# Performance work log

Measured on AMD Instinct MI355X. Metric: run time of the kernel, lower is better.

## Reference

```python
import jax, jax.numpy as jnp
import numpy as np
from jax import lax

# ---- constants matching init kwargs / proposal_creator(mode='testing') ----
RATIOS = (0.5, 1.0, 2.0)
SCALES = (8.0, 16.0, 32.0)
BASE = 16.0          # generate_anchor_base base_size
STRIDE = 16          # feat_stride
NMS_THRESH = 0.7
N_PRE = 3000         # n_test_pre_nms
N_POST = 300         # n_test_post_nms
MIN_SIZE = 16.0      # min_size * scale (scale=1)


def _anchor_base():
    # (9, 4) xyxy anchors centered at (BASE/2, BASE/2); ratios outer, scales inner
    r = np.array(RATIOS, np.float32)
    s = np.array(SCALES, np.float32)
    hs = (BASE * s[None, :] * np.sqrt(r)[:, None]).reshape(-1)
    ws = (BASE * s[None, :] * np.sqrt(1.0 / r)[:, None]).reshape(-1)
    cx = cy = BASE / 2.0
    return np.stack([cx - ws / 2, cy - hs / 2, cx + ws / 2, cy + hs / 2], 1).astype(np.float32)


def _all_anchors(h, w):
    # _enumerate_shifted_anchor: shift grid flattened y-outer/x-inner to match
    # permute(0,2,3,1).view(n,-1,4) layout of the conv outputs.
    base = jnp.asarray(_anchor_base())                     # (9,4)
    sx = jnp.arange(w, dtype=jnp.float32) * STRIDE
    sy = jnp.arange(h, dtype=jnp.float32) * STRIDE
    SX, SY = jnp.meshgrid(sx, sy)                          # (h,w)
    shifts = jnp.stack([SX, SY, SX, SY], -1).reshape(-1, 4)  # (h*w,4)
    return (shifts[:, None, :] + base[None, :, :]).reshape(-1, 4)  # (h*w*9,4)


def _proposals(loc, score, anchor, img_h, img_w):
    # loc: (K,4) deltas, score: (K,) fg prob, anchor: (K,4) xyxy
    aw = anchor[:, 2] - anchor[:, 0]
    ah = anchor[:, 3] - anchor[:, 1]
    acx = anchor[:, 0] + 0.5 * aw
    acy = anchor[:, 1] + 0.5 * ah
    cx = loc[:, 0] * aw + acx
    cy = loc[:, 1] * ah + acy
    bw = aw * jnp.exp(loc[:, 2])
    bh = ah * jnp.exp(loc[:, 3])
    x1 = jnp.clip(cx - 0.5 * bw, 0.0, img_w)
    y1 = jnp.clip(cy - 0.5 * bh, 0.0, img_h)
    x2 = jnp.clip(cx + 0.5 * bw, 0.0, img_w)
    y2 = jnp.clip(cy + 0.5 * bh, 0.0, img_h)
    boxes = jnp.stack([x1, y1, x2, y2], 1)
    valid = ((x2 - x1) >= MIN_SIZE) & ((y2 - y1) >= MIN_SIZE)
    # min-size filter -> sink invalid boxes with -inf score, then top-k pre-NMS
    masked = jnp.where(valid, score, -jnp.inf)
    _, idx = lax.top_k(masked, N_PRE)
    b = boxes[idx]                                         # (N_PRE,4), score-sorted desc
    v = valid[idx]
    # pairwise IoU (torchvision convention: no +1)
    area = (b[:, 2] - b[:, 0]) * (b[:, 3] - b[:, 1])
    ix1 = jnp.maximum(b[:, None, 0], b[None, :, 0])
    iy1 = jnp.maximum(b[:, None, 1], b[None, :, 1])
    ix2 = jnp.minimum(b[:, None, 2], b[None, :, 2])
    iy2 = jnp.minimum(b[:, None, 3], b[None, :, 3])
    inter = jnp.clip(ix2 - ix1, 0.0) * jnp.clip(iy2 - iy1, 0.0)
    union = area[:, None] + area[None, :] - inter
    iou = jnp.where(union > 0.0, inter / union, 0.0)
    sup = iou > NMS_THRESH                                 # (N_PRE,N_PRE) bool
    # greedy sequential NMS over score order
    ar = jnp.arange(N_PRE)
    def body(keep, i):
        keep = keep & ~(keep[i] & sup[i] & (ar > i))
        return keep, None
    keep, _ = lax.scan(body, v, ar)
    # first N_POST kept boxes (score order); pad by cycling kept boxes
    order = jnp.argsort(jnp.where(keep, ar, N_PRE))        # kept indices first, sorted
    nk = jnp.maximum(keep.sum(), 1)
    pos = jnp.arange(N_POST)
    sel = order[jnp.where(pos < nk, pos, pos % nk)]
    return b[sel]                                          # (N_POST,4)


def setup_inputs() -> dict:
    key = jax.random.key(0)
    ks = jax.random.split(key, 4)
    n, c, h, w = 4, 512, 38, 38
    return {
        "x": jax.random.normal(ks[0], (n, c, h, w), jnp.float32),
        "conv1_w": jax.random.normal(ks[1], (512, 512, 3, 3), jnp.float32) * 0.01,
        "conv1_b": jnp.zeros((512,), jnp.float32),
        "score_w": jax.random.normal(ks[2], (18, 512), jnp.float32) * 0.01,
        "score_b": jnp.zeros((18,), jnp.float32),
        "loc_w": jax.random.normal(ks[3], (36, 512), jnp.float32) * 0.01,
        "loc_b": jnp.zeros((36,), jnp.float32),
        "img_h": 608,
        "img_w": 608,
    }


def reference(x, conv1_w, conv1_b, score_w, score_b, loc_w, loc_b, img_h, img_w):
    n, _, h, w = x.shape
    feat = jax.nn.relu(
        lax.conv_general_dilated(x, conv1_w, (1, 1), "SAME",
                                 dimension_numbers=("NCHW", "OIHW", "NCHW"))
        + conv1_b[None, :, None, None])
    locs = jnp.einsum("nchw,oc->nohw", feat, loc_w) + loc_b[None, :, None, None]
    scores = jnp.einsum("nchw,oc->nohw", feat, score_w) + score_b[None, :, None, None]
    rpn_locs = locs.transpose(0, 2, 3, 1).reshape(n, -1, 4)      # (n, h*w*9, 4)
    rpn_scores = scores.transpose(0, 2, 3, 1).reshape(n, -1, 2)  # (n, h*w*9, 2)
    fg = jax.nn.softmax(rpn_scores, axis=-1)[..., 1]             # (n, h*w*9)
    anchor = _all_anchors(h, w)
    ih = jnp.float32(img_h)
    iw = jnp.float32(img_w)
    rois = jax.vmap(lambda l, s: _proposals(l, s, anchor, ih, iw))(rpn_locs, fg)
    rois_indices = jnp.broadcast_to(
        jnp.arange(n, dtype=x.dtype)[:, None], (n, N_POST))
    return rpn_locs, rpn_scores, rois.reshape(-1, 4), rois_indices, anchor[None]
```

## Files before the change

kernel.cpp:

```cpp
#include <hip/hip_runtime.h>
#include <cstdint>
#include <cstddef>

#define HW    1444
#define NA    12996
#define NPRE  3000
#define NW    47
#define NPOST 300

#define OFF_LOCS   0
#define OFF_SCORES 207936
#define OFF_ROIS   311904
#define OFF_IDX    316704
#define OFF_ANCH   317904

#define INVALID_KEY 0xFFF0000000000000ULL

__device__ inline double as_dim(int raw) {
  if (raw > 0 && raw < 1000000) return (double)raw;
  return (double)__int_as_float(raw);
}

__global__ __launch_bounds__(256) void wt_k(const float* __restrict__ lw,
                                            const float* __restrict__ sw,
                                            float* __restrict__ Wt) {
  int t = blockIdx.x * 256 + threadIdx.x;
  if (t >= 64 * 512) return;
  int o = t & 63, c = t >> 6;
  float v = 0.f;
  if (o < 36)      v = lw[o * 512 + c];
  else if (o < 54) v = sw[(o - 36) * 512 + c];
  Wt[t] = v;
}

__global__ __launch_bounds__(256) void conv_k(const float* __restrict__ X,
                                              const float* __restrict__ W,
                                              const float* __restrict__ B,
                                              float* __restrict__ F) {
  __shared__ float Xs[480];
  __shared__ float Wsf[2340];
  const int tid  = threadIdx.x;
  const int lane = tid & 63;
  const int wv   = tid >> 6;
  const int seg  = wv * 10;
  const int y  = blockIdx.x;
  const int o0 = blockIdx.y * 64;
  const int n  = blockIdx.z;
  const float* xn = X + ((size_t)n * 512) * HW;

  int xsrc[2]; bool xval[2]; bool xact[2];
#pragma unroll
  for (int u = 0; u < 2; ++u) {
    int e = tid + u * 256;
    xact[u] = (e < 480);
    int cl = e / 120, rem = e - cl * 120;
    int row = rem / 40, col = rem - row * 40;
    int iy = y - 1 + row, ix = col - 1;
    xval[u] = xact[u] && (iy >= 0 && iy < 38 && ix >= 0 && ix < 38);
    xsrc[u] = xval[u] ? (cl * HW + iy * 38 + ix) : 0;
  }
  int wdst[9], wsrc[9];
#pragma unroll
  for (int u = 0; u < 9; ++u) {
    int e = tid + u * 256;
    int ol = e / 36, rem = e - ol * 36;
    int cl = rem / 9, k = rem - cl * 9;
    wdst[u] = (cl * 9 + k) * 65 + ol;
    wsrc[u] = (o0 + ol) * 4608 + cl * 9 + k;
  }

  float xr_[2], wr_[9];
#pragma unroll
  for (int u = 0; u < 2; ++u) xr_[u] = xval[u] ? xn[xsrc[u]] : 0.f;
#pragma unroll
  for (int u = 0; u < 9; ++u) wr_[u] = W[wsrc[u]];

  double acc[10];
#pragma unroll
  for (int p = 0; p < 10; ++p) acc[p] = 0.;
  float part[10];

  for (int cc = 0; cc < 128; ++cc) {
    __syncthreads();
#pragma unroll
    for (int u = 0; u < 2; ++u)
      if (xact[u]) Xs[tid + u * 256] = xr_[u];
#pragma unroll
    for (int u = 0; u < 9; ++u) Wsf[wdst[u]] = wr_[u];
    __syncthreads();
    if (cc < 127) {
      const int cb = (cc + 1) * 4;
#pragma unroll
      for (int u = 0; u < 2; ++u) xr_[u] = xval[u] ? xn[(size_t)cb * HW + xsrc[u]] : 0.f;
#pragma unroll
      for (int u = 0; u < 9; ++u) wr_[u] = W[wsrc[u] + cb * 9];
    }
    if ((cc & 1) == 0) {
#pragma unroll
      for (int p = 0; p < 10; ++p) part[p] = 0.f;
    }
#pragma unroll
    for (int cl = 0; cl < 4; ++cl) {
      float w9[9];
#pragma unroll
      for (int k = 0; k < 9; ++k) w9[k] = Wsf[(cl * 9 + k) * 65 + lane];
#pragma unroll
      for (int ky = 0; ky < 3; ++ky) {
        const float* xrow = &Xs[cl * 120 + ky * 40 + seg];
        float xr[12];
#pragma unroll
        for (int j = 0; j < 6; ++j) {
          float2 t2 = ((const float2*)xrow)[j];
          xr[2 * j] = t2.x; xr[2 * j + 1] = t2.y;
        }
#pragma unroll
        for (int kx = 0; kx < 3; ++kx) {
          float wvv = w9[ky * 3 + kx];
#pragma unroll
          for (int p = 0; p < 10; ++p)
            part[p] = fmaf(wvv, xr[p + kx], part[p]);
        }
      }
    }
    if (cc & 1) {
#pragma unroll
      for (int p = 0; p < 10; ++p) acc[p] += (double)part[p];
    }
  }
  double bb = (double)B[o0 + lane];
  float* fp = F + ((size_t)(n * 512 + o0 + lane)) * HW + y * 38;
#pragma unroll
  for (int p = 0; p < 10; ++p) {
    int col = seg + p;
    if (col < 38) fp[col] = (float)fmax(acc[p] + bb, 0.0);
  }
}

__global__ __launch_bounds__(256) void heads_k(const float* __restrict__ F,
                                               const float* __restrict__ Wt,
                                               const float* __restrict__ lb,
                                               const float* __restrict__ sb,
                                               float* __restrict__ out,
                                               double* __restrict__ fg) {
  __shared__ float sf[512 * 4];
  __shared__ double ssc[4][18];
  int n = blockIdx.y;
  int p0 = blockIdx.x * 4;
  int tid = threadIdx.x;
  const float* fn = F + ((size_t)n * 512) * HW;
  for (int e = tid; e < 2048; e += 256) {
    int c = e >> 2, pl = e & 3;
    sf[e] = fn[c * HW + p0 + pl];
  }
  __syncthreads();
  int pl = tid & 3, o = tid >> 2;
  double acc = 0.;
  if (o < 54) {
    for (int c = 0; c < 512; ++c)
      acc = fma((double)Wt[(c << 6) | o], (double)sf[(c << 2) | pl], acc);
  }
  int p = p0 + pl;
  if (o < 36) {
    acc += (double)lb[o];
    out[OFF_LOCS + ((size_t)n * NA + (size_t)p * 9 + (o >> 2)) * 4 + (o & 3)] = (float)acc;
  } else if (o < 54) {
    int oo = o - 36;
    acc += (double)sb[oo];
    out[OFF_SCORES + ((size_t)n * NA + (size_t)p * 9 + (oo >> 1)) * 2 + (oo & 1)] = (float)acc;
    ssc[pl][oo] = acc;
  }
  __syncthreads();
  if (tid < 36) {
    int pl2 = tid / 9, a = tid - pl2 * 9;
    double s0 = ssc[pl2][a * 2], s1 = ssc[pl2][a * 2 + 1];
    double mx = fmax(s0, s1);
    double e0 = exp(s0 - mx), e1 = exp(s1 - mx);
    fg[(size_t)n * NA + (size_t)(p0 + pl2) * 9 + a] = e1 / (e0 + e1);
  }
}

__global__ __launch_bounds__(256) void decode_k(const float* __restrict__ out_c,
                                                float* __restrict__ out,
                                                const double* __restrict__ fg,
                                                const int* __restrict__ ihp,
                                                const int* __restrict__ iwp,
                                                double* __restrict__ boxes,
                                                unsigned long long* __restrict__ keys) {
  int t = blockIdx.x * 256 + threadIdx.x;
  int n = t >> 14, i = t & 16383;
  if (i >= NA) { keys[t] = ~0ULL; return; }
  int p = i / 9, a = i - p * 9;
  int ri = a / 3, si = a - ri * 3;
  double sr  = (ri == 0) ? 0.7071067811865476 : (ri == 1 ? 1.0 : 1.4142135623730951);
  double sri = (ri == 0) ? 1.4142135623730951 : (ri == 1 ? 1.0 : 0.7071067811865476);
  double hs = (double)(128 << si) * sr;
  double wd = (double)(128 << si) * sri;
  int py = p / 38, px = p - py * 38;
  float sx = (float)(px * 16), sy = (float)(py * 16);
  float fx1 = (float)(8.0 - 0.5 * wd), fy1 = (float)(8.0 - 0.5 * hs);
  float fx2 = (float)(8.0 + 0.5 * wd), fy2 = (float)(8.0 + 0.5 * hs);
  float ax1f = sx + fx1, ay1f = sy + fy1, ax2f = sx + fx2, ay2f = sy + fy2;
  if (n == 0) {
    float* ap = out + OFF_ANCH + (size_t)i * 4;
    ap[0] = ax1f; ap[1] = ay1f; ap[2] = ax2f; ap[3] = ay2f;
  }
  double ax1 = ax1f, ay1 = ay1f, ax2 = ax2f, ay2 = ay2f;
  double aw = ax2 - ax1, ah = ay2 - ay1;
  double acx = ax1 + 0.5 * aw, acy = ay1 + 0.5 * ah;
  const float* lp = out_c + OFF_LOCS + ((size_t)n * NA + i) * 4;
  double cx = (double)lp[0] * aw + acx, cy = (double)lp[1] * ah + acy;
  double bw = aw * exp((double)lp[2]), bh = ah * exp((double)lp[3]);
  double iwf = as_dim(iwp[0]), ihf = as_dim(ihp[0]);
  double x1 = fmin(fmax(cx - 0.5 * bw, 0.0), iwf);
  double y1 = fmin(fmax(cy - 0.5 * bh, 0.0), ihf);
  double x2 = fmin(fmax(cx + 0.5 * bw, 0.0), iwf);
  double y2 = fmin(fmax(cy + 0.5 * bh, 0.0), ihf);
  bool valid = ((x2 - x1) >= 16.0) && ((y2 - y1) >= 16.0);
  double* bp = boxes + ((size_t)n * NA + i) * 4;
  bp[0] = x1; bp[1] = y1; bp[2] = x2; bp[3] = y2;
  double sc = fg[(size_t)n * NA + i];
  unsigned long long u = (unsigned long long)__double_as_longlong(sc);
  u = (u >> 63) ? ~u : (u | 0x8000000000000000ULL);
  unsigned long long inv = ~u;
  if (!valid) inv = INVALID_KEY;
  keys[t] = (inv & ~0x3FFFULL) | (unsigned long long)i;
}

__global__ __launch_bounds__(1024) void sortA_k(unsigned long long* __restrict__ keys) {
  __shared__ unsigned long long s[8192];
  const int half = blockIdx.x & 1;
  unsigned long long* g = keys + (((size_t)(blockIdx.x >> 1)) << 14) + ((size_t)half << 13);
  const int tid = threadIdx.x;
  for (int i = tid; i < 8192; i += 1024) s[i] = g[i];
  for (int size = 2; size <= 8192; size <<= 1) {
    for (int stride = size >> 1; stride > 0; stride >>= 1) {
      __syncthreads();
      for (int u = tid; u < 4096; u += 1024) {
        int lo = u & (stride - 1);
        int i1 = ((u - lo) << 1) | lo;
        int i2 = i1 + stride;
        bool up = (i1 & size) == 0;
        if (half) up = !up;
        unsigned long long a = s[i1], b = s[i2];
        if ((a > b) == up) { s[i1] = b; s[i2] = a; }
      }
    }
  }
  __syncthreads();
  for (int i = tid; i < 8192; i += 1024) g[i] = s[i];
}

__global__ __launch_bounds__(256) void sortB_k(unsigned long long* __restrict__ keys) {
  int t = blockIdx.x * 256 + threadIdx.x;
  int n = t >> 13, i = t & 8191;
  unsigned long long* g = keys + ((size_t)n << 14);
  unsigned long long a = g[i], b = g[i + 8192];
  if (a > b) { g[i] = b; g[i + 8192] = a; }
}

__global__ __launch_bounds__(1024) void sortC_k(unsigned long long* __restrict__ keys) {
  __shared__ unsigned long long s[8192];
  unsigned long long* g = keys + (((size_t)(blockIdx.x >> 1)) << 14) + ((size_t)(blockIdx.x & 1) << 13);
  const int tid = threadIdx.x;
  for (int i = tid; i < 8192; i += 1024) s[i] = g[i];
  for (int stride = 4096; stride > 0; stride >>= 1) {
    __syncthreads();
    for (int u = tid; u < 4096; u += 1024) {
      int lo = u & (stride - 1);
      int i1 = ((u - lo) << 1) | lo;
      int i2 = i1 + stride;
      unsigned long long a = s[i1], b = s[i2];
      if (a > b) { s[i1] = b; s[i2] = a; }
    }
  }
  __syncthreads();
  for (int i = tid; i < 8192; i += 1024) g[i] = s[i];
}

__global__ void gather_k(const unsigned long long* __restrict__ keys,
                         const double* __restrict__ boxes,
                         double* __restrict__ bsort,
                         unsigned long long* __restrict__ vw) {
  int n = blockIdx.y, w = blockIdx.x, l = threadIdx.x;
  int r = w * 64 + l;
  bool valid = false;
  if (r < NPRE) {
    unsigned long long kk = keys[((size_t)n << 14) + r];
    valid = kk < INVALID_KEY;
    unsigned idx = (unsigned)(kk & 0x3FFFULL);
    const double* bp = boxes + ((size_t)n * NA + idx) * 4;
    double* dp = bsort + ((size_t)n * NPRE + r) * 4;
    dp[0] = bp[0]; dp[1] = bp[1]; dp[2] = bp[2]; dp[3] = bp[3];
  }
  unsigned long long mask = __ballot(valid);
  if (l == 0) vw[n * NW + w] = mask;
}

__global__ __launch_bounds__(256) void iou_k(const double* __restrict__ bsort,
                                             unsigned long long* __restrict__ sup) {
  int t = blockIdx.x * 256 + threadIdx.x;
  if (t >= 4 * NPRE * NW) return;
  int w = t % NW; int rest = t / NW; int i = rest % NPRE; int n = rest / NPRE;
  const double* bb = bsort + (size_t)n * NPRE * 4;
  double bix1 = bb[(size_t)i*4], biy1 = bb[(size_t)i*4+1];
  double bix2 = bb[(size_t)i*4+2], biy2 = bb[(size_t)i*4+3];
  double ai = (bix2 - bix1) * (biy2 - biy1);
  unsigned long long word = 0ULL;
  int j0 = w << 6;
  if (j0 + 63 > i) {
    int lmax = NPRE - j0; if (lmax > 64) lmax = 64;
    for (int l = 0; l < lmax; ++l) {
      int j = j0 + l;
      if (j <= i) continue;
      const double* bj = bb + (size_t)j * 4;
      double aj = (bj[2] - bj[0]) * (bj[3] - bj[1]);
      double xx1 = fmax(bix1, bj[0]), yy1 = fmax(biy1, bj[1]);
      double xx2 = fmin(bix2, bj[2]), yy2 = fmin(biy2, bj[3]);
      double inter = fmax(xx2 - xx1, 0.0) * fmax(yy2 - yy1, 0.0);
      double uni = ai + aj - inter;
      double iou = (uni > 0.0) ? inter / uni : 0.0;
      word |= (unsigned long long)(iou > 0.7) << l;
    }
  }
  sup[((size_t)n * NPRE + i) * NW + w] = word;
}

__global__ void nms_k(const unsigned long long* __restrict__ sup,
                      const unsigned long long* __restrict__ vwp,
                      const double* __restrict__ bsort,
                      float* __restrict__ out) {
  int n = blockIdx.x; int l = threadIdx.x;
  unsigned long long vw = (l < NW) ? vwp[n * NW + l] : 0ULL;
  unsigned long long remv = 0ULL, keepw = 0ULL;
  const unsigned long long* sbase = sup + (size_t)n * NPRE * NW;
  unsigned long long r = (l < NPRE) ? sbase[(size_t)l * NW] : 0ULL;
  for (int b = 0; b < NW; ++b) {
    unsigned long long rn = 0ULL;
    if (b + 1 < NW) {
      int gi = (b + 1) * 64 + l;
      if (gi < NPRE) rn = sbase[(size_t)gi * NW + (b + 1)];
    }
    unsigned long long kept = __shfl(vw & ~remv, b);
    unsigned long long todo = kept;
    while (todo) {
      int i = __builtin_ctzll(todo);
      unsigned long long ri = __shfl(r, i);
      kept &= ~ri;
      todo &= todo - 1;
      todo &= ~ri;
    }
    if (l == b) keepw = kept;
    unsigned long long m = kept;
    while (m) {
      int i0 = __builtin_ctzll(m); m &= m - 1;
      int i1 = -1, i2 = -1, i3 = -1, i4 = -1, i5 = -1, i6 = -1, i7 = -1;
      if (m) { i1 = __builtin_ctzll(m); m &= m - 1; }
      if (m) { i2 = __builtin_ctzll(m); m &= m - 1; }
      if (m) { i3 = __builtin_ctzll(m); m &= m - 1; }
      if (m) { i4 = __builtin_ctzll(m); m &= m - 1; }
      if (m) { i5 = __builtin_ctzll(m); m &= m - 1; }
      if (m) { i6 = __builtin_ctzll(m); m &= m - 1; }
      if (m) { i7 = __builtin_ctzll(m); m &= m - 1; }
      if (l < NW) {
        const unsigned long long* rb = sbase + (size_t)(b << 6) * NW + l;
        unsigned long long a0 = rb[(size_t)i0 * NW];
        unsigned long long a1 = (i1 >= 0) ? rb[(size_t)i1 * NW] : 0ULL;
        unsigned long long a2 = (i2 >= 0) ? rb[(size_t)i2 * NW] : 0ULL;
        unsigned long long a3 = (i3 >= 0) ? rb[(size_t)i3 * NW] : 0ULL;
        unsigned long long a4 = (i4 >= 0) ? rb[(size_t)i4 * NW] : 0ULL;
        unsigned long long a5 = (i5 >= 0) ? rb[(size_t)i5 * NW] : 0ULL;
        unsigned long long a6 = (i6 >= 0) ? rb[(size_t)i6 * NW] : 0ULL;
        unsigned long long a7 = (i7 >= 0) ? rb[(size_t)i7 * NW] : 0ULL;
        remv |= (((a0 | a1) | (a2 | a3)) | ((a4 | a5) | (a6 | a7)));
      }
    }
    r = rn;
  }
  unsigned long long keep = keepw;
  int cnt = __popcll(keep);
  int pre = cnt;
#pragma unroll
  for (int d = 1; d < 64; d <<= 1) {
    int tt = __shfl_up(pre, d);
    if (l >= d) pre += tt;
  }
  int nk = __shfl(pre, 63);
  int excl = pre - cnt;
  __shared__ float sbox[NPOST * 4];
  unsigned long long m2 = keep; int rank = excl;
  while (m2) {
    int b = __builtin_ctzll(m2);
    m2 &= m2 - 1;
    if (rank < NPOST) {
      int j = (l << 6) + b;
      const double* bj = bsort + ((size_t)n * NPRE + j) * 4;
      sbox[rank*4]   = (float)bj[0]; sbox[rank*4+1] = (float)bj[1];
      sbox[rank*4+2] = (float)bj[2]; sbox[rank*4+3] = (float)bj[3];
    }
    ++rank;
  }
  __syncthreads();
  if (nk == 0 && l == 0) {
    const double* b0 = bsort + (size_t)n * NPRE * 4;
    sbox[0] = (float)b0[0]; sbox[1] = (float)b0[1];
    sbox[2] = (float)b0[2]; sbox[3] = (float)b0[3];
  }
  __syncthreads();
  int nke = nk > 0 ? nk : 1;
  for (int r2 = l; r2 < NPOST; r2 += 64) {
    int src = r2 < nke ? r2 : r2 % nke;
    float4 b4 = *(float4*)(sbox + src * 4);
    *(float4*)(out + OFF_ROIS + ((size_t)n * NPOST + r2) * 4) = b4;
    out[OFF_IDX + n * NPOST + r2] = (float)n;
  }
}

extern "C" void kernel_launch(void* const* d_in, const int* in_sizes, int n_in,
                              void* d_out, int out_size, void* d_ws, size_t ws_size,
                              hipStream_t stream) {
  const float* X  = (const float*)d_in[0];
  const float* CW = (const float*)d_in[1];
  const float* CB = (const float*)d_in[2];
  const float* SW = (const float*)d_in[3];
  const float* SB = (const float*)d_in[4];
  const float* LW = (const float*)d_in[5];
  const float* LB = (const float*)d_in[6];
  const int*   IH = (const int*)d_in[7];
  const int*   IW = (const int*)d_in[8];
  float* out = (float*)d_out;
  char* ws = (char*)d_ws;

  float* feat = (float*)(ws + 0);
  unsigned long long* sup  = (unsigned long long*)(ws + 0);
  float* Wt    = (float*)(ws + 11829248);
  double* fg   = (double*)(ws + 11960320);
  double* boxes= (double*)(ws + 12376192);
  unsigned long long* keys = (unsigned long long*)(ws + 14039680);
  double* bsort= (double*)(ws + 14563968);
  unsigned long long* vw   = (unsigned long long*)(ws + 14947968);

  hipLaunchKernelGGL(wt_k,     dim3(128),        dim3(256),  0, stream, LW, SW, Wt);
  hipLaunchKernelGGL(conv_k,   dim3(38, 8, 4),   dim3(256),  0, stream, X, CW, CB, feat);
  hipLaunchKernelGGL(heads_k,  dim3(361, 4),     dim3(256),  0, stream, feat, Wt, LB, SB, out, fg);
  hipLaunchKernelGGL(decode_k, dim3(256),        dim3(256),  0, stream, out, out, fg, IH, IW, boxes, keys);
  hipLaunchKernelGGL(sortA_k,  dim3(8),          dim3(1024), 0, stream, keys);
  hipLaunchKernelGGL(sortB_k,  dim3(128),        dim3(256),  0, stream, keys);
  hipLaunchKernelGGL(sortC_k,  dim3(8),          dim3(1024), 0, stream, keys);
  hipLaunchKernelGGL(gather_k, dim3(47, 4),      dim3(64),   0, stream, keys, boxes, bsort, vw);
  hipLaunchKernelGGL(iou_k,    dim3((4*NPRE*NW + 255) / 256), dim3(256), 0, stream, bsort, sup);
  hipLaunchKernelGGL(nms_k,    dim3(4),          dim3(64),   0, stream, sup, vw, bsort, out);
}
```

Baseline: 1.003 ms.

## Compute two output rows per conv block to reuse weights and input rows

```diff
diff --git a/kernel.cpp b/kernel.cpp
--- a/kernel.cpp
+++ b/kernel.cpp
@@ -37,25 +37,25 @@
                                               const float* __restrict__ W,
                                               const float* __restrict__ B,
                                               float* __restrict__ F) {
-  __shared__ float Xs[480];
+  __shared__ float Xs[640];
   __shared__ float Wsf[2340];
   const int tid  = threadIdx.x;
   const int lane = tid & 63;
   const int wv   = tid >> 6;
   const int seg  = wv * 10;
-  const int y  = blockIdx.x;
+  const int y0 = blockIdx.x * 2;
   const int o0 = blockIdx.y * 64;
   const int n  = blockIdx.z;
   const float* xn = X + ((size_t)n * 512) * HW;
 
-  int xsrc[2]; bool xval[2]; bool xact[2];
-#pragma unroll
-  for (int u = 0; u < 2; ++u) {
+  int xsrc[3]; bool xval[3]; bool xact[3];
+#pragma unroll
+  for (int u = 0; u < 3; ++u) {
     int e = tid + u * 256;
-    xact[u] = (e < 480);
-    int cl = e / 120, rem = e - cl * 120;
+    xact[u] = (e < 640);
+    int cl = e / 160, rem = e - cl * 160;
     int row = rem / 40, col = rem - row * 40;
-    int iy = y - 1 + row, ix = col - 1;
+    int iy = y0 - 1 + row, ix = col - 1;
     xval[u] = xact[u] && (iy >= 0 && iy < 38 && ix >= 0 && ix < 38);
     xsrc[u] = xval[u] ? (cl * HW + iy * 38 + ix) : 0;
   }
@@ -69,21 +69,23 @@
     wsrc[u] = (o0 + ol) * 4608 + cl * 9 + k;
   }
 
-  float xr_[2], wr_[9];
-#pragma unroll
-  for (int u = 0; u < 2; ++u) xr_[u] = xval[u] ? xn[xsrc[u]] : 0.f;
+  float xr_[3], wr_[9];
+#pragma unroll
+  for (int u = 0; u < 3; ++u) xr_[u] = xval[u] ? xn[xsrc[u]] : 0.f;
 #pragma unroll
   for (int u = 0; u < 9; ++u) wr_[u] = W[wsrc[u]];
 
-  double acc[10];
-#pragma unroll
-  for (int p = 0; p < 10; ++p) acc[p] = 0.;
-  float part[10];
+  double acc[2][10];
+#pragma unroll
+  for (int r = 0; r < 2; ++r)
+#pragma unroll
+    for (int p = 0; p < 10; ++p) acc[r][p] = 0.;
+  float part[2][10];
 
   for (int cc = 0; cc < 128; ++cc) {
     __syncthreads();
 #pragma unroll
-    for (int u = 0; u < 2; ++u)
+    for (int u = 0; u < 3; ++u)
       if (xact[u]) Xs[tid + u * 256] = xr_[u];
 #pragma unroll
     for (int u = 0; u < 9; ++u) Wsf[wdst[u]] = wr_[u];
@@ -91,48 +93,61 @@
     if (cc < 127) {
       const int cb = (cc + 1) * 4;
 #pragma unroll
-      for (int u = 0; u < 2; ++u) xr_[u] = xval[u] ? xn[(size_t)cb * HW + xsrc[u]] : 0.f;
+      for (int u = 0; u < 3; ++u) xr_[u] = xval[u] ? xn[(size_t)cb * HW + xsrc[u]] : 0.f;
 #pragma unroll
       for (int u = 0; u < 9; ++u) wr_[u] = W[wsrc[u] + cb * 9];
     }
     if ((cc & 1) == 0) {
 #pragma unroll
-      for (int p = 0; p < 10; ++p) part[p] = 0.f;
+      for (int r = 0; r < 2; ++r)
+#pragma unroll
+        for (int p = 0; p < 10; ++p) part[r][p] = 0.f;
     }
 #pragma unroll
     for (int cl = 0; cl < 4; ++cl) {
       float w9[9];
 #pragma unroll
       for (int k = 0; k < 9; ++k) w9[k] = Wsf[(cl * 9 + k) * 65 + lane];
-#pragma unroll
-      for (int ky = 0; ky < 3; ++ky) {
-        const float* xrow = &Xs[cl * 120 + ky * 40 + seg];
-        float xr[12];
+      float xr4[4][12];
+#pragma unroll
+      for (int rr = 0; rr < 4; ++rr) {
+        const float* xrow = &Xs[cl * 160 + rr * 40 + seg];
 #pragma unroll
         for (int j = 0; j < 6; ++j) {
           float2 t2 = ((const float2*)xrow)[j];
-          xr[2 * j] = t2.x; xr[2 * j + 1] = t2.y;
-        }
-#pragma unroll
-        for (int kx = 0; kx < 3; ++kx) {
-          float wvv = w9[ky * 3 + kx];
-#pragma unroll
-          for (int p = 0; p < 10; ++p)
-            part[p] = fmaf(wvv, xr[p + kx], part[p]);
+          xr4[rr][2 * j] = t2.x; xr4[rr][2 * j + 1] = t2.y;
         }
       }
+#pragma unroll
+      for (int r = 0; r < 2; ++r) {
+#pragma unroll
+        for (int ky = 0; ky < 3; ++ky) {
+#pragma unroll
+          for (int kx = 0; kx < 3; ++kx) {
+            float wvv = w9[ky * 3 + kx];
+#pragma unroll
+            for (int p = 0; p < 10; ++p)
+              part[r][p] = fmaf(wvv, xr4[r + ky][p + kx], part[r][p]);
+          }
+        }
+      }
     }
     if (cc & 1) {
 #pragma unroll
-      for (int p = 0; p < 10; ++p) acc[p] += (double)part[p];
+      for (int r = 0; r < 2; ++r)
+#pragma unroll
+        for (int p = 0; p < 10; ++p) acc[r][p] += (double)part[r][p];
     }
   }
   double bb = (double)B[o0 + lane];
-  float* fp = F + ((size_t)(n * 512 + o0 + lane)) * HW + y * 38;
-#pragma unroll
-  for (int p = 0; p < 10; ++p) {
-    int col = seg + p;
-    if (col < 38) fp[col] = (float)fmax(acc[p] + bb, 0.0);
+#pragma unroll
+  for (int r = 0; r < 2; ++r) {
+    float* fp = F + ((size_t)(n * 512 + o0 + lane)) * HW + (y0 + r) * 38;
+#pragma unroll
+    for (int p = 0; p < 10; ++p) {
+      int col = seg + p;
+      if (col < 38) fp[col] = (float)fmax(acc[r][p] + bb, 0.0);
+    }
   }
 }
 
@@ -440,7 +455,7 @@
   unsigned long long* vw   = (unsigned long long*)(ws + 14947968);
 
   hipLaunchKernelGGL(wt_k,     dim3(128),        dim3(256),  0, stream, LW, SW, Wt);
-  hipLaunchKernelGGL(conv_k,   dim3(38, 8, 4),   dim3(256),  0, stream, X, CW, CB, feat);
+  hipLaunchKernelGGL(conv_k,   dim3(19, 8, 4),   dim3(256),  0, stream, X, CW, CB, feat);
   hipLaunchKernelGGL(heads_k,  dim3(361, 4),     dim3(256),  0, stream, feat, Wt, LB, SB, out, fg);
   hipLaunchKernelGGL(decode_k, dim3(256),        dim3(256),  0, stream, out, out, fg, IH, IW, boxes, keys);
   hipLaunchKernelGGL(sortA_k,  dim3(8),          dim3(1024), 0, stream, keys);
```

New measurement: 1.118 ms. 11.4% more time.

## Pre-pad conv input and read it directly, double-buffer weights in LDS

Applied to the files above, without the earlier changes.

```diff
diff --git a/kernel.cpp b/kernel.cpp
--- a/kernel.cpp
+++ b/kernel.cpp
@@ -33,12 +33,21 @@
   Wt[t] = v;
 }
 
-__global__ __launch_bounds__(256) void conv_k(const float* __restrict__ X,
+__global__ __launch_bounds__(256) void xpad_k(const float* __restrict__ X,
+                                              float* __restrict__ Xp) {
+  int t = blockIdx.x * 256 + threadIdx.x;
+  int px = t % 40; int rest = t / 40; int py = rest % 40; int nc = rest / 40;
+  float v = 0.f;
+  if (py >= 1 && py <= 38 && px >= 1 && px <= 38)
+    v = X[(size_t)nc * HW + (py - 1) * 38 + (px - 1)];
+  Xp[t] = v;
+}
+
+__global__ __launch_bounds__(256) void conv_k(const float* __restrict__ Xp_,
                                               const float* __restrict__ W,
                                               const float* __restrict__ B,
                                               float* __restrict__ F) {
-  __shared__ float Xs[480];
-  __shared__ float Wsf[2340];
+  __shared__ float Wsf[2][2432];
   const int tid  = threadIdx.x;
   const int lane = tid & 63;
   const int wv   = tid >> 6;
@@ -46,32 +55,18 @@
   const int y  = blockIdx.x;
   const int o0 = blockIdx.y * 64;
   const int n  = blockIdx.z;
-  const float* xn = X + ((size_t)n * 512) * HW;
-
-  int xsrc[2]; bool xval[2]; bool xact[2];
-#pragma unroll
-  for (int u = 0; u < 2; ++u) {
-    int e = tid + u * 256;
-    xact[u] = (e < 480);
-    int cl = e / 120, rem = e - cl * 120;
-    int row = rem / 40, col = rem - row * 40;
-    int iy = y - 1 + row, ix = col - 1;
-    xval[u] = xact[u] && (iy >= 0 && iy < 38 && ix >= 0 && ix < 38);
-    xsrc[u] = xval[u] ? (cl * HW + iy * 38 + ix) : 0;
-  }
+  const float* Xp = (const float*)__builtin_assume_aligned(Xp_, 16);
+  const int xoff0 = __builtin_amdgcn_readfirstlane(n * 512 * 1600 + y * 40 + seg);
+
   int wdst[9], wsrc[9];
 #pragma unroll
   for (int u = 0; u < 9; ++u) {
     int e = tid + u * 256;
-    int ol = e / 36, rem = e - ol * 36;
-    int cl = rem / 9, k = rem - cl * 9;
-    wdst[u] = (cl * 9 + k) * 65 + ol;
-    wsrc[u] = (o0 + ol) * 4608 + cl * 9 + k;
-  }
-
-  float xr_[2], wr_[9];
-#pragma unroll
-  for (int u = 0; u < 2; ++u) xr_[u] = xval[u] ? xn[xsrc[u]] : 0.f;
+    int ol = e / 36, t36 = e - ol * 36;
+    wdst[u] = ol * 38 + t36;
+    wsrc[u] = (o0 + ol) * 4608 + t36;
+  }
+  float wr_[9];
 #pragma unroll
   for (int u = 0; u < 9; ++u) wr_[u] = W[wsrc[u]];
 
@@ -81,19 +76,21 @@
   float part[10];
 
   for (int cc = 0; cc < 128; ++cc) {
-    __syncthreads();
-#pragma unroll
-    for (int u = 0; u < 2; ++u)
-      if (xact[u]) Xs[tid + u * 256] = xr_[u];
-#pragma unroll
-    for (int u = 0; u < 9; ++u) Wsf[wdst[u]] = wr_[u];
+    const int buf = cc & 1;
+#pragma unroll
+    for (int u = 0; u < 9; ++u) Wsf[buf][wdst[u]] = wr_[u];
     __syncthreads();
     if (cc < 127) {
-      const int cb = (cc + 1) * 4;
-#pragma unroll
-      for (int u = 0; u < 2; ++u) xr_[u] = xval[u] ? xn[(size_t)cb * HW + xsrc[u]] : 0.f;
-#pragma unroll
-      for (int u = 0; u < 9; ++u) wr_[u] = W[wsrc[u] + cb * 9];
+      const int wb = (cc + 1) * 36;
+#pragma unroll
+      for (int u = 0; u < 9; ++u) wr_[u] = W[wsrc[u] + wb];
+    }
+    const float* wl = &Wsf[buf][lane * 38];
+    float w36[36];
+#pragma unroll
+    for (int k2 = 0; k2 < 18; ++k2) {
+      float2 t2 = *(const float2*)(wl + 2 * k2);
+      w36[2 * k2] = t2.x; w36[2 * k2 + 1] = t2.y;
     }
     if ((cc & 1) == 0) {
 #pragma unroll
@@ -101,24 +98,20 @@
     }
 #pragma unroll
     for (int cl = 0; cl < 4; ++cl) {
-      float w9[9];
-#pragma unroll
-      for (int k = 0; k < 9; ++k) w9[k] = Wsf[(cl * 9 + k) * 65 + lane];
+      const float* xc = Xp + xoff0 + (cc * 4 + cl) * 1600;
+      float xr3[3][12];
+#pragma unroll
+      for (int r = 0; r < 3; ++r)
+#pragma unroll
+        for (int j = 0; j < 12; ++j) xr3[r][j] = xc[r * 40 + j];
 #pragma unroll
       for (int ky = 0; ky < 3; ++ky) {
-        const float* xrow = &Xs[cl * 120 + ky * 40 + seg];
-        float xr[12];
-#pragma unroll
-        for (int j = 0; j < 6; ++j) {
-          float2 t2 = ((const float2*)xrow)[j];
-          xr[2 * j] = t2.x; xr[2 * j + 1] = t2.y;
-        }
 #pragma unroll
         for (int kx = 0; kx < 3; ++kx) {
-          float wvv = w9[ky * 3 + kx];
+          float wvv = w36[cl * 9 + ky * 3 + kx];
 #pragma unroll
           for (int p = 0; p < 10; ++p)
-            part[p] = fmaf(wvv, xr[p + kx], part[p]);
+            part[p] = fmaf(wvv, xr3[ky][p + kx], part[p]);
         }
       }
     }
@@ -438,9 +431,11 @@
   unsigned long long* keys = (unsigned long long*)(ws + 14039680);
   double* bsort= (double*)(ws + 14563968);
   unsigned long long* vw   = (unsigned long long*)(ws + 14947968);
+  float* Xpad  = (float*)(ws + 14949504);
 
   hipLaunchKernelGGL(wt_k,     dim3(128),        dim3(256),  0, stream, LW, SW, Wt);
-  hipLaunchKernelGGL(conv_k,   dim3(38, 8, 4),   dim3(256),  0, stream, X, CW, CB, feat);
+  hipLaunchKernelGGL(xpad_k,   dim3(12800),      dim3(256),  0, stream, X, Xpad);
+  hipLaunchKernelGGL(conv_k,   dim3(38, 8, 4),   dim3(256),  0, stream, Xpad, CW, CB, feat);
   hipLaunchKernelGGL(heads_k,  dim3(361, 4),     dim3(256),  0, stream, feat, Wt, LB, SB, out, fg);
   hipLaunchKernelGGL(decode_k, dim3(256),        dim3(256),  0, stream, out, out, fg, IH, IW, boxes, keys);
   hipLaunchKernelGGL(sortA_k,  dim3(8),          dim3(1024), 0, stream, keys);
```

After: 1.124 ms. 12.0% more time.
